# Kernel tuning notes

Hardware: AMD Instinct MI355X
Metric: run time of the kernel (lower is better)

The kernel has to match this reference:

```python
import jax, jax.numpy as jnp
import numpy as np

G = 8
K = 3  # kernel size; Unfold uses padding=1, stride=1 -> output same HxW


def _unfold3x3(x):
    # x: (b, c, h, w) -> (b, c, K*K, h, w), patch order (kh, kw) matching torch Unfold
    b, c, h, w = x.shape
    xp = jnp.pad(x, ((0, 0), (0, 0), (1, 1), (1, 1)))
    patches = [xp[:, :, i:i + h, j:j + w] for i in range(K) for j in range(K)]
    return jnp.stack(patches, axis=2)


def setup_inputs() -> dict:
    key = jax.random.key(0)
    k1, k2, k3, k4, k5 = jax.random.split(key, 5)
    b, c, h, w = 16, 256, 56, 56
    r = 2
    return {
        "x": jax.random.normal(k1, (b, c, h, w), dtype=jnp.float32),
        "w_reduce": jax.random.normal(k2, (c // r, c), dtype=jnp.float32) * (1.0 / np.sqrt(c)),
        "b_reduce": jax.random.normal(k3, (c // r,), dtype=jnp.float32) * 0.01,
        "w_span": jax.random.normal(k4, (K * K * G, c // r), dtype=jnp.float32) * (1.0 / np.sqrt(c // r)),
        "b_span": jax.random.normal(k5, (K * K * G,), dtype=jnp.float32) * 0.01,
    }


def reference(x, w_reduce, b_reduce, w_span, b_span):
    b, c, h, w = x.shape
    kk = K * K
    # dynamic kernel: two 1x1 convs (ss=1 -> no pooling)
    red = jnp.einsum('bchw,oc->bohw', x, w_reduce) + b_reduce[None, :, None, None]
    ker = jnp.einsum('bohw,ko->bkhw', red, w_span) + b_span[None, :, None, None]
    ker = ker.reshape(b, G, kk, h, w)
    # unfold: (b, c, kk, h, w) -> (b, G, c//G, kk, h, w)
    xu = _unfold3x3(x).reshape(b, G, c // G, kk, h, w)
    # broadcast-mul and reduce over kernel positions
    out = jnp.einsum('bgkhw,bgdkhw->bgdhw', ker, xu)
    return out.reshape(b, c, h, w)
```

## Files before the change

### kernel.cpp

```cpp
#include <hip/hip_runtime.h>
#include <hip/hip_bf16.h>

#define HW 3136
#define CC 256
#define MM 72
#define HH 56
#define WW 56

typedef __attribute__((ext_vector_type(8))) short short8;
typedef __attribute__((ext_vector_type(4))) float f32x4;

#define WAITVM(n) asm volatile("s_waitcnt vmcnt(" #n ")" ::: "memory")

__device__ __forceinline__ void blockbar() {
    asm volatile("" ::: "memory");
    __builtin_amdgcn_s_barrier();
    asm volatile("" ::: "memory");
}

__device__ inline unsigned short f2b(float f) {
    unsigned u; __builtin_memcpy(&u, &f, 4);
    unsigned r = u + 0x7fffu + ((u >> 16) & 1u);
    return (unsigned short)(r >> 16);
}
__device__ inline float b2f(unsigned short s) {
    unsigned u = ((unsigned)s) << 16; float f; __builtin_memcpy(&f, &u, 4);
    return f;
}
__device__ __forceinline__ unsigned short f2b_native(float f) {
    __hip_bfloat16 h = __float2bfloat16(f);
    unsigned short s; __builtin_memcpy(&s, &h, 2);
    return s;
}

__device__ __forceinline__ void gl2lds16(const float* g, float* l) {
    __builtin_amdgcn_global_load_lds(
        (const __attribute__((address_space(1))) void*)g,
        (__attribute__((address_space(3))) void*)l, 16, 0, 0);
}

__global__ __launch_bounds__(256) void k0_combine(
    const float* __restrict__ w_reduce,
    const float* __restrict__ b_reduce,
    const float* __restrict__ w_span,
    const float* __restrict__ b_span,
    unsigned short* __restrict__ wbf,
    float* __restrict__ bcomb)
{
    __shared__ float red[4][64];
    __shared__ float redb[256];

    const int m  = blockIdx.x;
    const int cq = blockIdx.y;
    const int t  = threadIdx.x;
    const int oq = t >> 6;
    const int cl = t & 63;
    const int c  = cq * 64 + cl;

    float acc = 0.f;
    if (m < MM) {
        const float* wsB = w_span   + m * 128 + oq * 32;
        const float* wrB = w_reduce + (size_t)(oq * 32) * 256 + c;
#pragma unroll 8
        for (int o = 0; o < 32; ++o)
            acc = fmaf(wsB[o], wrB[(size_t)o * 256], acc);
    }
    if (oq != 0) red[oq][cl] = acc;
    __syncthreads();
    if (oq == 0)
        wbf[m * 256 + c] = f2b(acc + red[1][cl] + red[2][cl] + red[3][cl]);

    if (cq == 0) {
        redb[t] = (m < MM && t < 128) ? w_span[m * 128 + t] * b_reduce[t] : 0.f;
        __syncthreads();
#pragma unroll
        for (int s2 = 128; s2 > 0; s2 >>= 1) {
            if (t < s2) redb[t] += redb[t + s2];
            __syncthreads();
        }
        if (t == 0) bcomb[m] = (m < MM ? b_span[m] : 0.f) + redb[0];
    }
}

__global__ __launch_bounds__(448, 4) void k_fused(
    const float* __restrict__ x,
    const unsigned short* __restrict__ wbf,
    const float* __restrict__ bcomb,
    float* __restrict__ out)
{
    __shared__ __align__(16) float xsb[3 * 3584];
    __shared__ __align__(16) unsigned short wsl[3][2560];
    __shared__ __align__(16) unsigned short kl[MM * 112];

    const int L   = blockIdx.x;
    const int wk  = (L & 7) * 56 + (L >> 3);
    const int b   = wk / 28;
    const int rem = wk - b * 28;
    const int ht  = rem >> 1;
    const int cs  = rem & 1;
    const int h0  = ht * 4;
    const int c0  = cs * 28;

    const int t    = threadIdx.x;
    const int lane = t & 63;
    const int wv   = t >> 6;
    const int l15  = lane & 15;
    const int q    = lane >> 4;

    const int chh   = t / 28;
    const int rem28 = t - chh * 28;
    const int rA    = rem28 / 7;
    const int qA    = rem28 - rA * 7;

    const float* xb = x + (size_t)b * CC * HW;

    const int nb   = wv * 16 + l15;
    const int nb2  = q * 112 + nb;
    const int swA  = (l15 ^ (l15 >> 2)) & 3;
    const int aBo  = l15 * 32 + (q ^ swA) * 8;
    const int cA   = ((chh & 3) << 3) | (chh >> 2);
    const int pxo  = (h0 + rA) * WW + c0 + qA * 4;
    const int wswr = ((t >> 2) ^ (t >> 4)) & 3;
    const unsigned short* wsrc0 = wbf + (t >> 2) * 256 + ((t & 3) ^ wswr) * 8;

    int boff[2];
#pragma unroll
    for (int i = 0; i < 2; ++i) {
        const int f  = i * 448 + t;
        const int fc = f < 864 ? f : 863;
        const int d  = fc / 54;
        const int r2 = fc - d * 54;
        const int rr = r2 / 9;
        const int qd = r2 - rr * 9;
        const int hh = h0 - 1 + rr;
        const int hc = hh < 0 ? 0 : (hh > 55 ? 55 : hh);
        int colc = c0 - 4 + qd * 4;
        colc = colc < 0 ? 0 : (colc > 52 ? 52 : colc);
        boff[i] = d * HW + hc * WW + colc;
    }

    float vmm[3];
#pragma unroll
    for (int kh = 0; kh < 3; ++kh) {
        const int row = h0 + rA - 1 + kh;
        vmm[kh] = (row >= 0 && row < HH) ? 1.f : 0.f;
    }
    const float lm  = (cs == 0 && qA == 0) ? 0.f : 1.f;
    const float rmm = (cs == 1 && qA == 6) ? 0.f : 1.f;

    auto stageX = [&](int s) {
        const float* sp = xb + (size_t)(s * 32 + cA) * HW + pxo;
        float* dp = xsb + (s % 3) * 3584 + t * 4;
        gl2lds16(sp, dp);
        gl2lds16(sp + (size_t)4 * HW, dp + 1792);
    };
    auto stageW = [&](int s) {
        if (t < 320)
            gl2lds16((const float*)(wsrc0 + s * 32), (float*)(wsl[s % 3]) + t * 4);
    };
    auto stageB = [&](int c) {
        const float* gp = xb + (size_t)(c * 16) * HW;
        float* dp = xsb + ((8 + c) % 3) * 3584;
        gl2lds16(gp + boff[0], dp + t * 4);
        gl2lds16(gp + boff[1], dp + (448 + t) * 4);
    };

    f32x4 acc[5];
#pragma unroll
    for (int mt = 0; mt < 5; ++mt)
#pragma unroll
        for (int r = 0; r < 4; ++r)
            acc[mt][r] = bcomb[mt * 16 + q * 4 + r];

    stageX(0); stageW(0);
    stageX(1); stageW(1);
    stageX(2); stageW(2);

#pragma unroll 1
    for (int p = 0; p < 8; ++p) {
        if (p < 6)      { if (t < 320) WAITVM(6); else WAITVM(4); }
        else if (p == 6){ if (t < 320) WAITVM(5); else WAITVM(4); }
        else            { WAITVM(4); }
        blockbar();

        const float* bufA = xsb + (p % 3) * 3584;
        const unsigned short* wp = wsl[p % 3];
        union { short8 v; unsigned short u16[8]; } bq;
#pragma unroll
        for (int j = 0; j < 8; ++j)
            bq.u16[j] = f2b_native(bufA[nb2 + j * 448]);
#pragma unroll
        for (int mt = 0; mt < 5; ++mt) {
            const short8 aq = *(const short8*)&wp[mt * 512 + aBo];
            acc[mt] = __builtin_amdgcn_mfma_f32_16x16x32_bf16(aq, bq.v, acc[mt], 0, 0, 0);
        }
        if (p == 7) {
#pragma unroll
            for (int mt = 0; mt < 5; ++mt)
#pragma unroll
                for (int r = 0; r < 4; ++r) {
                    const int m = mt * 16 + q * 4 + r;
                    if (m < MM) kl[m * 112 + nb] = f2b(acc[mt][r]);
                }
            asm volatile("s_waitcnt lgkmcnt(0)" ::: "memory");
        }
        blockbar();
        if (p <= 4) { stageX(p + 3); stageW(p + 3); }
        else        { stageB(p - 5); }
    }

    f32x4 kr[9];
#pragma unroll 1
    for (int g2 = 0; g2 < 16; ++g2) {
        if (g2 == 0)       WAITVM(4);
        else if (g2 == 1)  WAITVM(5);
        else if (g2 <= 13) WAITVM(6);
        else if (g2 == 14) WAITVM(4);
        else               WAITVM(2);
        blockbar();

        if ((g2 & 1) == 0) {
            const int g = g2 >> 1;
            ushort4 krb[9];
#pragma unroll
            for (int kk = 0; kk < 9; ++kk)
                krb[kk] = *(const ushort4*)&kl[(g * 9 + kk) * 112 + rA * 28 + qA * 4];
#pragma unroll
            for (int kh = 0; kh < 3; ++kh) {
#pragma unroll
                for (int j = 0; j < 3; ++j) {
                    const int kk = kh * 3 + j;
                    kr[kk].x = b2f(krb[kk].x) * vmm[kh];
                    kr[kk].y = b2f(krb[kk].y) * vmm[kh];
                    kr[kk].z = b2f(krb[kk].z) * vmm[kh];
                    kr[kk].w = b2f(krb[kk].w) * vmm[kh];
                }
                kr[kh * 3 + 0].x *= lm;
                kr[kh * 3 + 2].w *= rmm;
            }
        }

        const float* bp = xsb + ((8 + g2) % 3) * 3584 + chh * 216;
        f32x4 a = {0.f, 0.f, 0.f, 0.f};
#pragma unroll
        for (int kh = 0; kh < 3; ++kh) {
            const float* rowp = bp + (rA + kh) * 36;
            const f32x4 q0v = *(const f32x4*)(rowp + qA * 4);
            const f32x4 q1v = *(const f32x4*)(rowp + qA * 4 + 4);
            const float tl  = rowp[qA * 4 + 8];
            const float w0 = q0v.w, w1 = q1v.x, w2 = q1v.y,
                        w3 = q1v.z, w4 = q1v.w, w5 = tl;
            const f32x4 k0v = kr[kh * 3 + 0];
            const f32x4 k1v = kr[kh * 3 + 1];
            const f32x4 k2v = kr[kh * 3 + 2];
            a.x = fmaf(k0v.x, w0, a.x); a.y = fmaf(k0v.y, w1, a.y);
            a.z = fmaf(k0v.z, w2, a.z); a.w = fmaf(k0v.w, w3, a.w);
            a.x = fmaf(k1v.x, w1, a.x); a.y = fmaf(k1v.y, w2, a.y);
            a.z = fmaf(k1v.z, w3, a.z); a.w = fmaf(k1v.w, w4, a.w);
            a.x = fmaf(k2v.x, w2, a.x); a.y = fmaf(k2v.y, w3, a.y);
            a.z = fmaf(k2v.z, w4, a.z); a.w = fmaf(k2v.w, w5, a.w);
        }
        float* ob = out + ((size_t)b * CC + g2 * 16 + chh) * HW
                  + (h0 + rA) * WW + c0 + qA * 4;
        *(f32x4*)ob = a;

        blockbar();
        if (g2 <= 12) stageB(g2 + 3);
    }
}

extern "C" void kernel_launch(void* const* d_in, const int* in_sizes, int n_in,
                              void* d_out, int out_size, void* d_ws, size_t ws_size,
                              hipStream_t stream) {
    const float* x        = (const float*)d_in[0];
    const float* w_reduce = (const float*)d_in[1];
    const float* b_reduce = (const float*)d_in[2];
    const float* w_span   = (const float*)d_in[3];
    const float* b_span   = (const float*)d_in[4];
    float* out = (float*)d_out;

    char* ws = (char*)d_ws;
    unsigned short* wbf   = (unsigned short*)ws;
    float*          bcomb = (float*)(ws + 40960);

    k0_combine<<<dim3(80, 4), 256, 0, stream>>>(w_reduce, b_reduce, w_span, b_span,
                                                wbf, bcomb);
    k_fused<<<dim3(448), 448, 0, stream>>>(x, wbf, bcomb, out);
}
```

Before: 38.82 us.

## Read involution neighborhoods directly from global memory instead of LDS staging

Drops the LDS-staged, barrier-synchronised pipeline for the unfold/aggregation phase. Each thread now loads its 3x3 neighborhood straight from global memory (through cache), using clamped row and column indices, and handles two channels per group iteration. This removes the per-step block barriers and async LDS copies, and the wait counts in the first loop change to match. The cost is more global and L2 traffic from overlapping neighborhood reads, plus scalar edge loads, with no overlap from prefetching.

```diff
diff --git a/kernel.cpp b/kernel.cpp
--- a/kernel.cpp
+++ b/kernel.cpp
@@ -123,30 +123,19 @@
     const int wswr = ((t >> 2) ^ (t >> 4)) & 3;
     const unsigned short* wsrc0 = wbf + (t >> 2) * 256 + ((t & 3) ^ wswr) * 8;
 
-    int boff[2];
-#pragma unroll
-    for (int i = 0; i < 2; ++i) {
-        const int f  = i * 448 + t;
-        const int fc = f < 864 ? f : 863;
-        const int d  = fc / 54;
-        const int r2 = fc - d * 54;
-        const int rr = r2 / 9;
-        const int qd = r2 - rr * 9;
-        const int hh = h0 - 1 + rr;
-        const int hc = hh < 0 ? 0 : (hh > 55 ? 55 : hh);
-        int colc = c0 - 4 + qd * 4;
-        colc = colc < 0 ? 0 : (colc > 52 ? 52 : colc);
-        boff[i] = d * HW + hc * WW + colc;
-    }
-
     float vmm[3];
+    int   hcB[3];
 #pragma unroll
     for (int kh = 0; kh < 3; ++kh) {
         const int row = h0 + rA - 1 + kh;
         vmm[kh] = (row >= 0 && row < HH) ? 1.f : 0.f;
+        hcB[kh] = row < 0 ? 0 : (row > 55 ? 55 : row);
     }
     const float lm  = (cs == 0 && qA == 0) ? 0.f : 1.f;
     const float rmm = (cs == 1 && qA == 6) ? 0.f : 1.f;
+    const int colB = c0 + qA * 4;
+    const int wl   = (lm  == 0.f) ? colB : colB - 1;
+    const int wr   = (rmm == 0.f) ? 55   : colB + 4;
 
     auto stageX = [&](int s) {
         const float* sp = xb + (size_t)(s * 32 + cA) * HW + pxo;
@@ -158,12 +147,6 @@
         if (t < 320)
             gl2lds16((const float*)(wsrc0 + s * 32), (float*)(wsl[s % 3]) + t * 4);
     };
-    auto stageB = [&](int c) {
-        const float* gp = xb + (size_t)(c * 16) * HW;
-        float* dp = xsb + ((8 + c) % 3) * 3584;
-        gl2lds16(gp + boff[0], dp + t * 4);
-        gl2lds16(gp + boff[1], dp + (448 + t) * 4);
-    };
 
     f32x4 acc[5];
 #pragma unroll
@@ -179,8 +162,8 @@
 #pragma unroll 1
     for (int p = 0; p < 8; ++p) {
         if (p < 6)      { if (t < 320) WAITVM(6); else WAITVM(4); }
-        else if (p == 6){ if (t < 320) WAITVM(5); else WAITVM(4); }
-        else            { WAITVM(4); }
+        else if (p == 6){ if (t < 320) WAITVM(3); else WAITVM(2); }
+        else            { WAITVM(0); }
         blockbar();
 
         const float* bufA = xsb + (p % 3) * 3584;
@@ -206,66 +189,55 @@
         }
         blockbar();
         if (p <= 4) { stageX(p + 3); stageW(p + 3); }
-        else        { stageB(p - 5); }
-    }
-
-    f32x4 kr[9];
+    }
+
 #pragma unroll 1
-    for (int g2 = 0; g2 < 16; ++g2) {
-        if (g2 == 0)       WAITVM(4);
-        else if (g2 == 1)  WAITVM(5);
-        else if (g2 <= 13) WAITVM(6);
-        else if (g2 == 14) WAITVM(4);
-        else               WAITVM(2);
-        blockbar();
-
-        if ((g2 & 1) == 0) {
-            const int g = g2 >> 1;
-            ushort4 krb[9];
-#pragma unroll
-            for (int kk = 0; kk < 9; ++kk)
-                krb[kk] = *(const ushort4*)&kl[(g * 9 + kk) * 112 + rA * 28 + qA * 4];
+    for (int gg = 0; gg < 8; ++gg) {
+        ushort4 krb[9];
+#pragma unroll
+        for (int kk = 0; kk < 9; ++kk)
+            krb[kk] = *(const ushort4*)&kl[(gg * 9 + kk) * 112 + rA * 28 + qA * 4];
+
+        f32x4 kr[9];
+#pragma unroll
+        for (int kh = 0; kh < 3; ++kh) {
+#pragma unroll
+            for (int j = 0; j < 3; ++j) {
+                const int kk = kh * 3 + j;
+                kr[kk].x = b2f(krb[kk].x) * vmm[kh];
+                kr[kk].y = b2f(krb[kk].y) * vmm[kh];
+                kr[kk].z = b2f(krb[kk].z) * vmm[kh];
+                kr[kk].w = b2f(krb[kk].w) * vmm[kh];
+            }
+            kr[kh * 3 + 0].x *= lm;
+            kr[kh * 3 + 2].w *= rmm;
+        }
+
+        float* ob = out + ((size_t)b * CC + gg * 32 + chh * 2) * HW
+                  + (h0 + rA) * WW + colB;
+#pragma unroll
+        for (int dd = 0; dd < 2; ++dd) {
+            const float* base = xb + (size_t)(gg * 32 + chh * 2 + dd) * HW;
+            f32x4 a = {0.f, 0.f, 0.f, 0.f};
 #pragma unroll
             for (int kh = 0; kh < 3; ++kh) {
-#pragma unroll
-                for (int j = 0; j < 3; ++j) {
-                    const int kk = kh * 3 + j;
-                    kr[kk].x = b2f(krb[kk].x) * vmm[kh];
-                    kr[kk].y = b2f(krb[kk].y) * vmm[kh];
-                    kr[kk].z = b2f(krb[kk].z) * vmm[kh];
-                    kr[kk].w = b2f(krb[kk].w) * vmm[kh];
-                }
-                kr[kh * 3 + 0].x *= lm;
-                kr[kh * 3 + 2].w *= rmm;
+                const float* rowp = base + hcB[kh] * WW;
+                const f32x4 q1v = *(const f32x4*)(rowp + colB);
+                const float w0 = rowp[wl];
+                const float w5 = rowp[wr];
+                const float w1 = q1v.x, w2 = q1v.y, w3 = q1v.z, w4 = q1v.w;
+                const f32x4 k0v = kr[kh * 3 + 0];
+                const f32x4 k1v = kr[kh * 3 + 1];
+                const f32x4 k2v = kr[kh * 3 + 2];
+                a.x = fmaf(k0v.x, w0, a.x); a.y = fmaf(k0v.y, w1, a.y);
+                a.z = fmaf(k0v.z, w2, a.z); a.w = fmaf(k0v.w, w3, a.w);
+                a.x = fmaf(k1v.x, w1, a.x); a.y = fmaf(k1v.y, w2, a.y);
+                a.z = fmaf(k1v.z, w3, a.z); a.w = fmaf(k1v.w, w4, a.w);
+                a.x = fmaf(k2v.x, w2, a.x); a.y = fmaf(k2v.y, w3, a.y);
+                a.z = fmaf(k2v.z, w4, a.z); a.w = fmaf(k2v.w, w5, a.w);
             }
-        }
-
-        const float* bp = xsb + ((8 + g2) % 3) * 3584 + chh * 216;
-        f32x4 a = {0.f, 0.f, 0.f, 0.f};
-#pragma unroll
-        for (int kh = 0; kh < 3; ++kh) {
-            const float* rowp = bp + (rA + kh) * 36;
-            const f32x4 q0v = *(const f32x4*)(rowp + qA * 4);
-            const f32x4 q1v = *(const f32x4*)(rowp + qA * 4 + 4);
-            const float tl  = rowp[qA * 4 + 8];
-            const float w0 = q0v.w, w1 = q1v.x, w2 = q1v.y,
-                        w3 = q1v.z, w4 = q1v.w, w5 = tl;
-            const f32x4 k0v = kr[kh * 3 + 0];
-            const f32x4 k1v = kr[kh * 3 + 1];
-            const f32x4 k2v = kr[kh * 3 + 2];
-            a.x = fmaf(k0v.x, w0, a.x); a.y = fmaf(k0v.y, w1, a.y);
-            a.z = fmaf(k0v.z, w2, a.z); a.w = fmaf(k0v.w, w3, a.w);
-            a.x = fmaf(k1v.x, w1, a.x); a.y = fmaf(k1v.y, w2, a.y);
-            a.z = fmaf(k1v.z, w3, a.z); a.w = fmaf(k1v.w, w4, a.w);
-            a.x = fmaf(k2v.x, w2, a.x); a.y = fmaf(k2v.y, w3, a.y);
-            a.z = fmaf(k2v.z, w4, a.z); a.w = fmaf(k2v.w, w5, a.w);
-        }
-        float* ob = out + ((size_t)b * CC + g2 * 16 + chh) * HW
-                  + (h0 + rA) * WW + c0 + qA * 4;
-        *(f32x4*)ob = a;
-
-        blockbar();
-        if (g2 <= 12) stageB(g2 + 3);
+            *(f32x4*)(ob + (size_t)dd * HW) = a;
+        }
     }
 }
 
```

After: 49.73 us. 1.28x slower.
